# Kernel optimization log

Hardware: AMD Instinct MI355X
Metric: run time of the kernel (lower is better)

Reference implementation:

```python
import jax, jax.numpy as jnp
import numpy as np

N, E = 10000, 320000
NODE_DIM, EDGE_DIM, HID, H, L = 128, 64, 128, 4, 2
NEG_SLOPE = 0.2
BN_EPS = 1e-5


def setup_inputs() -> dict:
    key = jax.random.key(0)
    ks = jax.random.split(key, 20)
    s = 0.05
    return {
        "x": jax.random.normal(ks[0], (N, NODE_DIM), jnp.float32),
        "edge_index": jax.random.randint(ks[1], (2, E), 0, N, jnp.int32),
        "edge_attr": jax.random.normal(ks[2], (E, EDGE_DIM), jnp.float32),
        "batch": jnp.zeros((N,), jnp.int32),
        "enc_W": jax.random.normal(ks[3], (NODE_DIM, HID), jnp.float32) * s,
        "enc_b": jnp.zeros((HID,), jnp.float32),
        "eenc_W": jax.random.normal(ks[4], (EDGE_DIM, HID), jnp.float32) * s,
        "eenc_b": jnp.zeros((HID,), jnp.float32),
        "W": jax.random.normal(ks[5], (L, HID, H * HID), jnp.float32) * s,
        "We": jax.random.normal(ks[6], (L, HID, H * HID), jnp.float32) * s,
        "att_src": jax.random.normal(ks[7], (L, H, HID), jnp.float32) * s,
        "att_dst": jax.random.normal(ks[8], (L, H, HID), jnp.float32) * s,
        "att_edge": jax.random.normal(ks[9], (L, H, HID), jnp.float32) * s,
        "bias": jnp.zeros((L, HID), jnp.float32),
        "gamma": jnp.ones((L, HID), jnp.float32),
        "beta": jnp.zeros((L, HID), jnp.float32),
    }


def _forward(x, edge_attr, enc_W, enc_b, eenc_W, eenc_b, W, We,
             att_src, att_dst, att_edge, bias, gamma, beta, src, dst):
    h = x @ enc_W + enc_b                      # [N, HID]
    ea = edge_attr @ eenc_W + eenc_b           # [E, HID]
    # add self-loops; fill_value='mean' -> per-dst-node mean of incoming edge feats
    deg = jax.ops.segment_sum(jnp.ones((E,), ea.dtype), dst, N)          # [N]
    loop_attr = jax.ops.segment_sum(ea, dst, N) / jnp.maximum(deg, 1.0)[:, None]
    src_f = jnp.concatenate([src, jnp.arange(N, dtype=src.dtype)])       # [E+N]
    dst_f = jnp.concatenate([dst, jnp.arange(N, dtype=dst.dtype)])
    ea_f = jnp.concatenate([ea, loop_attr], axis=0)                      # [E+N, HID]

    for l in range(L):
        xh = (h @ W[l]).reshape(N, H, HID)                 # [N,H,C]
        eh = (ea_f @ We[l]).reshape(E + N, H, HID)         # [E+N,H,C]
        a_src = jnp.einsum('nhc,hc->nh', xh, att_src[l])   # [N,H]
        a_dst = jnp.einsum('nhc,hc->nh', xh, att_dst[l])
        a_e = jnp.einsum('ehc,hc->eh', eh, att_edge[l])    # [E+N,H]
        alpha = a_src[src_f] + a_dst[dst_f] + a_e
        alpha = jnp.where(alpha >= 0, alpha, NEG_SLOPE * alpha)  # leaky_relu
        amax = jax.ops.segment_max(alpha, dst_f, N)        # [N,H]
        alpha = jnp.exp(alpha - amax[dst_f])
        denom = jax.ops.segment_sum(alpha, dst_f, N)       # [N,H]
        alpha = alpha / (denom[dst_f] + 1e-16)
        msg = xh[src_f] * alpha[:, :, None]                # [E+N,H,C]
        out = jax.ops.segment_sum(msg, dst_f, N).mean(axis=1) + bias[l]  # concat=False -> head mean
        mu = out.mean(axis=0)
        var = out.var(axis=0)
        out = (out - mu) * jax.lax.rsqrt(var + BN_EPS) * gamma[l] + beta[l]
        h = jax.nn.relu(out) + h                           # relu, dropout(eval)=id, residual
    return h


def reference(x, edge_index, edge_attr, batch, enc_W, enc_b, eenc_W, eenc_b,
              W, We, att_src, att_dst, att_edge, bias, gamma, beta):
    src, dst = edge_index[0], edge_index[1]
    return _forward(x, edge_attr, enc_W, enc_b, eenc_W, eenc_b, W, We,
                    att_src, att_dst, att_edge, bias, gamma, beta, src, dst)
```

## Files before the change

kernel.cpp:

```cpp
#include <hip/hip_runtime.h>
#include <hip/hip_bf16.h>

typedef __attribute__((ext_vector_type(8))) short short8;
typedef __attribute__((ext_vector_type(4))) float f32x4;

__device__ __forceinline__ unsigned short f2bf(float x) {
    unsigned int u = __float_as_uint(x);
    u += 0x7fffu + ((u >> 16) & 1u);
    return (unsigned short)(u >> 16);
}

__device__ __forceinline__ unsigned int pack2(float a, float b) {
    return (unsigned int)f2bf(a) | ((unsigned int)f2bf(b) << 16);
}

__device__ __forceinline__ float2 bf2(unsigned int u) {
    float lo = __uint_as_float(u << 16);
    float hi = __uint_as_float(u & 0xffff0000u);
    return make_float2(lo, hi);
}

__global__ __launch_bounds__(256) void k_prep(const float* __restrict__ encW,
                                              const float* __restrict__ W,
                                              unsigned short* __restrict__ encWT16,
                                              unsigned short* __restrict__ WT16) {
    int o = blockIdx.x * 256 + threadIdx.x;
    if (o < 16384) {
        int c = o >> 7, k = o & 127;
        encWT16[o] = f2bf(encW[k * 128 + c]);
    } else if (o < 16384 + 131072) {
        int o2 = o - 16384;
        int l = o2 >> 16, r = o2 & 65535;
        int c = r >> 7, k = r & 127;
        WT16[o2] = f2bf(W[((size_t)l * 128 + k) * 512 + c]);
    }
}

__global__ __launch_bounds__(256) void k_wa(const float* __restrict__ W,
                                            const float* __restrict__ We,
                                            const float* __restrict__ att_src,
                                            const float* __restrict__ att_dst,
                                            const float* __restrict__ att_edge,
                                            float* __restrict__ we_att,
                                            float* __restrict__ wa_sd) {
    int o = blockIdx.x * 256 + threadIdx.x;
    if (o < 1024) {
        int k = o >> 3, lh = o & 7, l = lh >> 2, h = lh & 3;
        const float* wrow = We + ((size_t)(l * 128 + k)) * 512 + h * 128;
        const float* av = att_edge + (l * 4 + h) * 128;
        float s = 0.f;
        #pragma unroll 8
        for (int c = 0; c < 128; ++c) s = fmaf(wrow[c], av[c], s);
        we_att[o] = s;
    } else if (o < 3072) {
        int o2 = o - 1024;
        int l = o2 >> 10, r = o2 & 1023, k = r >> 3, m = r & 7, h = m & 3;
        const float* wrow = W + ((size_t)(l * 128 + k)) * 512 + h * 128;
        const float* av = (m < 4 ? att_src : att_dst) + (l * 4 + h) * 128;
        float s = 0.f;
        #pragma unroll 8
        for (int c = 0; c < 128; ++c) s = fmaf(wrow[c], av[c], s);
        wa_sd[o2] = s;
    }
}

__global__ __launch_bounds__(256) void k_mw(const float* __restrict__ eencW,
                                            const float* __restrict__ eencb,
                                            const float* __restrict__ we_att,
                                            float* __restrict__ MW,
                                            float* __restrict__ cvec) {
    int o = blockIdx.x * 256 + threadIdx.x;
    if (o < 512) {
        int k = o >> 3, q = o & 7;
        float s = 0.f;
        #pragma unroll 8
        for (int c = 0; c < 128; ++c) s = fmaf(eencW[k * 128 + c], we_att[c * 8 + q], s);
        MW[o] = s;
    } else if (o < 520) {
        int q = o - 512;
        float s = 0.f;
        #pragma unroll 8
        for (int c = 0; c < 128; ++c) s = fmaf(eencb[c], we_att[c * 8 + q], s);
        cvec[q] = s;
    }
}

template <int NC, bool A32, bool W32, bool W16, bool BIAS>
__global__ __launch_bounds__(256) void k_gemm_mfma(
    const void* __restrict__ A,
    const unsigned short* __restrict__ BT16,
    const float* __restrict__ bias,
    float* __restrict__ C,
    unsigned short* __restrict__ C16, int M) {
    __shared__ unsigned short a_lds[64][136];
    __shared__ unsigned short b_lds[64][136];
    int t = threadIdx.x;
    int rbase = blockIdx.x * 64;
    int cbase = blockIdx.y * 64;
    #pragma unroll
    for (int i = 0; i < 4; ++i) {
        int idx = t * 8 + i * 2048;
        int r = idx >> 7, k = idx & 127;
        if constexpr (A32) {
            const float* Af = (const float*)A;
            float4 f0 = make_float4(0.f, 0.f, 0.f, 0.f), f1 = f0;
            if (rbase + r < M) {
                f0 = *(const float4*)(Af + (size_t)(rbase + r) * 128 + k);
                f1 = *(const float4*)(Af + (size_t)(rbase + r) * 128 + k + 4);
            }
            uint4 v = make_uint4(pack2(f0.x, f0.y), pack2(f0.z, f0.w),
                                 pack2(f1.x, f1.y), pack2(f1.z, f1.w));
            *(uint4*)&a_lds[r][k] = v;
        } else {
            const unsigned short* Ah = (const unsigned short*)A;
            uint4 v = make_uint4(0u, 0u, 0u, 0u);
            if (rbase + r < M) v = *(const uint4*)(Ah + (size_t)(rbase + r) * 128 + k);
            *(uint4*)&a_lds[r][k] = v;
        }
    }
    #pragma unroll
    for (int i = 0; i < 4; ++i) {
        int idx = t * 8 + i * 2048;
        int r = idx >> 7, k = idx & 127;
        uint4 v = *(const uint4*)(BT16 + (size_t)(cbase + r) * 128 + k);
        *(uint4*)&b_lds[r][k] = v;
    }
    __syncthreads();
    int lane = t & 63, w = t >> 6;
    int lr = lane & 15, lk = (lane >> 4) * 8;
    f32x4 acc[4] = {f32x4{0.f, 0.f, 0.f, 0.f}, f32x4{0.f, 0.f, 0.f, 0.f},
                    f32x4{0.f, 0.f, 0.f, 0.f}, f32x4{0.f, 0.f, 0.f, 0.f}};
    #pragma unroll
    for (int kt = 0; kt < 4; ++kt) {
        short8 a = *(const short8*)&a_lds[w * 16 + lr][kt * 32 + lk];
        #pragma unroll
        for (int ct = 0; ct < 4; ++ct) {
            short8 b = *(const short8*)&b_lds[ct * 16 + lr][kt * 32 + lk];
            acc[ct] = __builtin_amdgcn_mfma_f32_16x16x32_bf16(a, b, acc[ct], 0, 0, 0);
        }
    }
    int rw = rbase + w * 16 + (lane >> 4) * 4;
    #pragma unroll
    for (int ct = 0; ct < 4; ++ct) {
        int col = cbase + ct * 16 + lr;
        float bv = 0.f;
        if constexpr (BIAS) bv = bias[col];
        #pragma unroll
        for (int j = 0; j < 4; ++j) {
            int r = rw + j;
            if (r < M) {
                float v = acc[ct][j] + bv;
                if constexpr (W32) C[(size_t)r * NC + col] = v;
                if constexpr (W16) C16[(size_t)r * NC + col] = f2bf(v);
            }
        }
    }
}

__global__ __launch_bounds__(256) void k_hist(const int* __restrict__ dst,
                                              int* __restrict__ deg, int E_) {
    int e = blockIdx.x * 256 + threadIdx.x;
    if (e < E_) atomicAdd(&deg[dst[e]], 1);
}

__global__ __launch_bounds__(1024) void k_scan(const int* __restrict__ deg,
                                               int* __restrict__ offs, int n) {
    __shared__ int part[1024];
    int t = threadIdx.x;
    int per = (n + 1023) / 1024;
    int beg = t * per, end = min(beg + per, n);
    int s = 0;
    for (int i = beg; i < end; ++i) s += deg[i];
    part[t] = s;
    __syncthreads();
    for (int off = 1; off < 1024; off <<= 1) {
        int v = (t >= off) ? part[t - off] : 0;
        __syncthreads();
        part[t] += v;
        __syncthreads();
    }
    int run = (t == 0) ? 0 : part[t - 1];
    for (int i = beg; i < end; ++i) { offs[i] = run; run += deg[i]; }
    if (t == 1023) offs[n] = run;
}

__global__ __launch_bounds__(256) void k_fill_ae(
    const int* __restrict__ dst, const int* __restrict__ src,
    const int* __restrict__ offs, int* __restrict__ fill,
    const float* __restrict__ eattr, const float* __restrict__ MW,
    const float* __restrict__ cvec,
    int* __restrict__ src_s, float* __restrict__ a_e_i, int E_) {
    __shared__ float mw[64][8];
    __shared__ float cv[8];
    int t = threadIdx.x;
    for (int i = t; i < 512; i += 256) mw[i >> 3][i & 7] = MW[i];
    if (t < 8) cv[t] = cvec[t];
    __syncthreads();
    int e = blockIdx.x * 256 + t;
    if (e >= E_) return;
    float acc[8];
    #pragma unroll
    for (int q = 0; q < 8; ++q) acc[q] = cv[q];
    const float4* r = (const float4*)(eattr + (size_t)e * 64);
    #pragma unroll 4
    for (int k4 = 0; k4 < 16; ++k4) {
        float4 v = r[k4];
        float xc[4] = {v.x, v.y, v.z, v.w};
        #pragma unroll
        for (int m = 0; m < 4; ++m)
            #pragma unroll
            for (int q = 0; q < 8; ++q)
                acc[q] = fmaf(xc[m], mw[k4 * 4 + m][q], acc[q]);
    }
    int d = dst[e];
    int pos = offs[d] + atomicAdd(&fill[d], 1);
    src_s[pos] = src[e];
    *(float4*)(a_e_i + (size_t)pos * 8) = make_float4(acc[0], acc[1], acc[2], acc[3]);
    *(float4*)(a_e_i + (size_t)pos * 8 + 4) = make_float4(acc[4], acc[5], acc[6], acc[7]);
}

__global__ __launch_bounds__(256) void k_rowdot8(const float* __restrict__ X,
                                                 const float* __restrict__ V,
                                                 float* __restrict__ O, int M) {
    __shared__ float v_lds[128][8];
    int t = threadIdx.x;
    for (int idx = t; idx < 1024; idx += 256) v_lds[idx >> 3][idx & 7] = V[idx];
    __syncthreads();
    int row = blockIdx.x * 256 + t;
    if (row >= M) return;
    float acc[8] = {};
    const float4* x4 = (const float4*)(X + (size_t)row * 128);
    for (int k4 = 0; k4 < 32; ++k4) {
        float4 xv = x4[k4];
        float xc[4] = {xv.x, xv.y, xv.z, xv.w};
        #pragma unroll
        for (int m = 0; m < 4; ++m)
            #pragma unroll
            for (int o = 0; o < 8; ++o) acc[o] = fmaf(xc[m], v_lds[k4 * 4 + m][o], acc[o]);
    }
    *(float4*)(O + (size_t)row * 8) = make_float4(acc[0], acc[1], acc[2], acc[3]);
    *(float4*)(O + (size_t)row * 8 + 4) = make_float4(acc[4], acc[5], acc[6], acc[7]);
}

__global__ __launch_bounds__(256) void k_agg(
    const int* __restrict__ offs, const int* __restrict__ src_s,
    const float* __restrict__ a_sd, const float* __restrict__ a_e_i,
    const unsigned short* __restrict__ xh16,
    float* __restrict__ outb, int N_, int lsel) {
    int wid = (blockIdx.x * 256 + threadIdx.x) >> 6;
    int lane = threadIdx.x & 63;
    if (wid >= N_) return;
    int n = wid;
    int s0 = offs[n], s1 = offs[n + 1];
    int hsel = lane >> 4;
    int qoff = lsel * 4 + hsel;
    float ad = a_sd[(size_t)n * 8 + 4 + hsel];
    float acc[8] = {};
    float ssum = 0.f, macc = 0.f;
    int sn_next = (s0 < s1) ? src_s[s0] : 0;
    for (int idx = s0; idx < s1; ++idx) {
        int sn = sn_next;
        if (idx + 1 < s1) sn_next = src_s[idx + 1];
        float ae = a_e_i[(size_t)idx * 8 + qoff];
        float as = a_sd[(size_t)sn * 8 + hsel];
        uint4 v = *(const uint4*)(xh16 + (size_t)sn * 512 + lane * 8);
        macc += ae;
        float raw = as + ae + ad;
        raw = raw >= 0.f ? raw : 0.2f * raw;
        float ex = __expf(raw);
        ssum += ex;
        float2 p0 = bf2(v.x), p1 = bf2(v.y), p2 = bf2(v.z), p3 = bf2(v.w);
        acc[0] = fmaf(ex, p0.x, acc[0]); acc[1] = fmaf(ex, p0.y, acc[1]);
        acc[2] = fmaf(ex, p1.x, acc[2]); acc[3] = fmaf(ex, p1.y, acc[3]);
        acc[4] = fmaf(ex, p2.x, acc[4]); acc[5] = fmaf(ex, p2.y, acc[5]);
        acc[6] = fmaf(ex, p3.x, acc[6]); acc[7] = fmaf(ex, p3.y, acc[7]);
    }
    {
        float dg = (float)max(s1 - s0, 1);
        float ae = macc / dg;
        float as = a_sd[(size_t)n * 8 + hsel];
        float raw = as + ae + ad;
        raw = raw >= 0.f ? raw : 0.2f * raw;
        float ex = __expf(raw);
        ssum += ex;
        uint4 v = *(const uint4*)(xh16 + (size_t)n * 512 + lane * 8);
        float2 p0 = bf2(v.x), p1 = bf2(v.y), p2 = bf2(v.z), p3 = bf2(v.w);
        acc[0] = fmaf(ex, p0.x, acc[0]); acc[1] = fmaf(ex, p0.y, acc[1]);
        acc[2] = fmaf(ex, p1.x, acc[2]); acc[3] = fmaf(ex, p1.y, acc[3]);
        acc[4] = fmaf(ex, p2.x, acc[4]); acc[5] = fmaf(ex, p2.y, acc[5]);
        acc[6] = fmaf(ex, p3.x, acc[6]); acc[7] = fmaf(ex, p3.y, acc[7]);
    }
    float inv = 0.25f / (ssum + 1e-16f);
    #pragma unroll
    for (int q = 0; q < 8; ++q) acc[q] *= inv;
    #pragma unroll
    for (int off = 16; off <= 32; off <<= 1)
        #pragma unroll
        for (int q = 0; q < 8; ++q) acc[q] += __shfl_xor(acc[q], off);
    if (lane < 16) {
        float* orow = outb + (size_t)n * 128 + lane * 8;
        *(float4*)orow = make_float4(acc[0], acc[1], acc[2], acc[3]);
        *(float4*)(orow + 4) = make_float4(acc[4], acc[5], acc[6], acc[7]);
    }
}

__global__ __launch_bounds__(128) void k_bnstats(const float* __restrict__ outb,
                                                 float* __restrict__ bnsum,
                                                 float* __restrict__ bnsumsq, int N_) {
    int c = threadIdx.x;
    float s = 0.f, s2 = 0.f;
    for (int r = blockIdx.x; r < N_; r += gridDim.x) {
        float v = outb[(size_t)r * 128 + c];
        s += v;
        s2 = fmaf(v, v, s2);
    }
    atomicAdd(&bnsum[c], s);
    atomicAdd(&bnsumsq[c], s2);
}

template <bool DOROW>
__global__ __launch_bounds__(256) void k_bn_apply_rd(
    const float* __restrict__ outb, const float* __restrict__ bnsum,
    const float* __restrict__ bnsumsq, const float* __restrict__ gamma,
    const float* __restrict__ beta, const float* __restrict__ wa,
    float* __restrict__ h, unsigned short* __restrict__ h16,
    float* __restrict__ a_sd, int N_) {
    __shared__ float wlds[128][8];
    int t = threadIdx.x;
    if constexpr (DOROW) {
        for (int i = t; i < 1024; i += 256) wlds[i >> 3][i & 7] = wa[i];
        __syncthreads();
    }
    int wid = (blockIdx.x * 256 + t) >> 6;
    int lane = t & 63;
    if (wid >= N_) return;
    int n = wid;
    float invN = 1.0f / (float)N_;
    int c0 = lane, c1 = lane + 64;
    float mu0 = bnsum[c0] * invN, mu1 = bnsum[c1] * invN;
    float g0 = rsqrtf(bnsumsq[c0] * invN - mu0 * mu0 + 1e-5f) * gamma[c0];
    float g1 = rsqrtf(bnsumsq[c1] * invN - mu1 * mu1 + 1e-5f) * gamma[c1];
    float o0 = outb[(size_t)n * 128 + c0], o1 = outb[(size_t)n * 128 + c1];
    float v0 = (o0 - mu0) * g0 + beta[c0];
    float v1 = (o1 - mu1) * g1 + beta[c1];
    float nh0 = h[(size_t)n * 128 + c0] + fmaxf(v0, 0.f);
    float nh1 = h[(size_t)n * 128 + c1] + fmaxf(v1, 0.f);
    h[(size_t)n * 128 + c0] = nh0;
    h[(size_t)n * 128 + c1] = nh1;
    h16[(size_t)n * 128 + c0] = f2bf(nh0);
    h16[(size_t)n * 128 + c1] = f2bf(nh1);
    if constexpr (DOROW) {
        float p[8];
        #pragma unroll
        for (int m = 0; m < 8; ++m)
            p[m] = fmaf(nh0, wlds[c0][m], nh1 * wlds[c1][m]);
        #pragma unroll
        for (int off = 1; off < 64; off <<= 1)
            #pragma unroll
            for (int m = 0; m < 8; ++m) p[m] += __shfl_xor(p[m], off);
        if (lane == 0) {
            *(float4*)(a_sd + (size_t)n * 8) = make_float4(p[0], p[1], p[2], p[3]);
            *(float4*)(a_sd + (size_t)n * 8 + 4) = make_float4(p[4], p[5], p[6], p[7]);
        }
    }
}

extern "C" void kernel_launch(void* const* d_in, const int* in_sizes, int n_in,
                              void* d_out, int out_size, void* d_ws, size_t ws_size,
                              hipStream_t stream) {
    const float* x = (const float*)d_in[0];
    const int* ei = (const int*)d_in[1];
    const float* eattr = (const float*)d_in[2];
    const float* encW = (const float*)d_in[4];
    const float* encb = (const float*)d_in[5];
    const float* eencW = (const float*)d_in[6];
    const float* eencb = (const float*)d_in[7];
    const float* W = (const float*)d_in[8];
    const float* We = (const float*)d_in[9];
    const float* att_src = (const float*)d_in[10];
    const float* att_dst = (const float*)d_in[11];
    const float* att_edge = (const float*)d_in[12];
    const float* gamma = (const float*)d_in[14];
    const float* beta = (const float*)d_in[15];

    const int N = in_sizes[0] / 128;
    const int E = in_sizes[1] / 2;
    const int* srcIdx = ei;
    const int* dstIdx = ei + E;
    float* h = (float*)d_out;

    char* wbase = (char*)d_ws;
    size_t off = 0;
    auto alloc = [&](size_t bytes) -> void* {
        void* p = wbase + off;
        off = (off + bytes + 255) & ~(size_t)255;
        return p;
    };
    unsigned short* encWT16 = (unsigned short*)alloc((size_t)128 * 128 * 2);
    unsigned short* WT16 = (unsigned short*)alloc((size_t)2 * 512 * 128 * 2);
    float* we_att = (float*)alloc((size_t)128 * 8 * 4);
    float* wa_sd = (float*)alloc((size_t)2 * 128 * 8 * 4);
    float* MW = (float*)alloc((size_t)64 * 8 * 4);
    float* cvec = (float*)alloc((size_t)8 * 4);
    int* deg = (int*)alloc((size_t)2 * N * 4);
    int* fill = deg + N;
    int* offs = (int*)alloc((size_t)(N + 1) * 4);
    int* src_s = (int*)alloc((size_t)E * 4);
    float* a_e_i = (float*)alloc((size_t)E * 8 * 4);
    float* a_sd = (float*)alloc((size_t)N * 8 * 4);
    unsigned short* h16 = (unsigned short*)alloc((size_t)N * 128 * 2);
    unsigned short* xh16 = (unsigned short*)alloc((size_t)N * 512 * 2);
    float* outb = (float*)alloc((size_t)N * 128 * 4);
    float* bnsum = (float*)alloc((size_t)4 * 128 * 4);
    float* bnsumsq = bnsum + 2 * 128;
    (void)ws_size; (void)n_in; (void)out_size;

    hipMemsetAsync(deg, 0, (size_t)2 * N * 4, stream);
    hipMemsetAsync(bnsum, 0, (size_t)4 * 128 * 4, stream);

    k_prep<<<(16384 + 131072 + 255) / 256, 256, 0, stream>>>(encW, W, encWT16, WT16);
    k_wa<<<12, 256, 0, stream>>>(W, We, att_src, att_dst, att_edge, we_att, wa_sd);
    k_mw<<<3, 256, 0, stream>>>(eencW, eencb, we_att, MW, cvec);

    k_gemm_mfma<128, true, true, true, true>
        <<<dim3((N + 63) / 64, 2), 256, 0, stream>>>(x, encWT16, encb, h, h16, N);

    int eb = (E + 255) / 256;
    k_hist<<<eb, 256, 0, stream>>>(dstIdx, deg, E);
    k_scan<<<1, 1024, 0, stream>>>(deg, offs, N);
    k_fill_ae<<<eb, 256, 0, stream>>>(dstIdx, srcIdx, offs, fill, eattr, MW, cvec,
                                      src_s, a_e_i, E);

    k_rowdot8<<<(N + 255) / 256, 256, 0, stream>>>(h, wa_sd, a_sd, N);

    int ab = (N * 64 + 255) / 256;
    for (int l = 0; l < 2; ++l) {
        k_gemm_mfma<512, false, false, true, false>
            <<<dim3((N + 63) / 64, 8), 256, 0, stream>>>(
                h16, WT16 + (size_t)l * 512 * 128, nullptr, nullptr, xh16, N);
        k_agg<<<ab, 256, 0, stream>>>(
            offs, src_s, a_sd, a_e_i, xh16, outb, N, l);
        k_bnstats<<<256, 128, 0, stream>>>(outb, bnsum + l * 128, bnsumsq + l * 128, N);
        if (l == 0) {
            k_bn_apply_rd<true><<<ab, 256, 0, stream>>>(
                outb, bnsum, bnsumsq, gamma, beta, wa_sd + 1024, h, h16, a_sd, N);
        } else {
            k_bn_apply_rd<false><<<ab, 256, 0, stream>>>(
                outb, bnsum + 128, bnsumsq + 128, gamma + 128, beta + 128,
                nullptr, h, h16, nullptr, N);
        }
    }
}
```

Measured before the change: 272.0 us.

## Merge setup kernels into fewer launches and unroll aggregation loop by two

Combines the weight prep, attention-weight folding and degree histogram into one launch, runs the scan alongside the MW computation in a two-block launch, and merges edge fill with the source/dest row dot into one launch. This removes several small kernel launches and the gaps between them. The aggregation loop now handles two edges per iteration with separate accumulators, which raises memory-level parallelism at the cost of more registers.

```diff
diff --git a/kernel.cpp b/kernel.cpp
--- a/kernel.cpp
+++ b/kernel.cpp
@@ -20,69 +20,90 @@
     return make_float2(lo, hi);
 }
 
-__global__ __launch_bounds__(256) void k_prep(const float* __restrict__ encW,
-                                              const float* __restrict__ W,
-                                              unsigned short* __restrict__ encWT16,
-                                              unsigned short* __restrict__ WT16) {
-    int o = blockIdx.x * 256 + threadIdx.x;
-    if (o < 16384) {
-        int c = o >> 7, k = o & 127;
-        encWT16[o] = f2bf(encW[k * 128 + c]);
-    } else if (o < 16384 + 131072) {
-        int o2 = o - 16384;
-        int l = o2 >> 16, r = o2 & 65535;
-        int c = r >> 7, k = r & 127;
-        WT16[o2] = f2bf(W[((size_t)l * 128 + k) * 512 + c]);
-    }
-}
-
-__global__ __launch_bounds__(256) void k_wa(const float* __restrict__ W,
-                                            const float* __restrict__ We,
-                                            const float* __restrict__ att_src,
-                                            const float* __restrict__ att_dst,
-                                            const float* __restrict__ att_edge,
-                                            float* __restrict__ we_att,
-                                            float* __restrict__ wa_sd) {
-    int o = blockIdx.x * 256 + threadIdx.x;
-    if (o < 1024) {
-        int k = o >> 3, lh = o & 7, l = lh >> 2, h = lh & 3;
-        const float* wrow = We + ((size_t)(l * 128 + k)) * 512 + h * 128;
-        const float* av = att_edge + (l * 4 + h) * 128;
-        float s = 0.f;
-        #pragma unroll 8
-        for (int c = 0; c < 128; ++c) s = fmaf(wrow[c], av[c], s);
-        we_att[o] = s;
-    } else if (o < 3072) {
-        int o2 = o - 1024;
-        int l = o2 >> 10, r = o2 & 1023, k = r >> 3, m = r & 7, h = m & 3;
-        const float* wrow = W + ((size_t)(l * 128 + k)) * 512 + h * 128;
-        const float* av = (m < 4 ? att_src : att_dst) + (l * 4 + h) * 128;
-        float s = 0.f;
-        #pragma unroll 8
-        for (int c = 0; c < 128; ++c) s = fmaf(wrow[c], av[c], s);
-        wa_sd[o2] = s;
-    }
-}
-
-__global__ __launch_bounds__(256) void k_mw(const float* __restrict__ eencW,
-                                            const float* __restrict__ eencb,
-                                            const float* __restrict__ we_att,
-                                            float* __restrict__ MW,
-                                            float* __restrict__ cvec) {
-    int o = blockIdx.x * 256 + threadIdx.x;
-    if (o < 512) {
-        int k = o >> 3, q = o & 7;
-        float s = 0.f;
-        #pragma unroll 8
-        for (int c = 0; c < 128; ++c) s = fmaf(eencW[k * 128 + c], we_att[c * 8 + q], s);
-        MW[o] = s;
-    } else if (o < 520) {
-        int q = o - 512;
-        float s = 0.f;
-        #pragma unroll 8
-        for (int c = 0; c < 128; ++c) s = fmaf(eencb[c], we_att[c * 8 + q], s);
-        cvec[q] = s;
-    }
+__global__ __launch_bounds__(256) void k_misc1(
+    const float* __restrict__ encW, const float* __restrict__ W,
+    const float* __restrict__ We, const float* __restrict__ att_src,
+    const float* __restrict__ att_dst, const float* __restrict__ att_edge,
+    const int* __restrict__ dst,
+    unsigned short* __restrict__ encWT16, unsigned short* __restrict__ WT16,
+    float* __restrict__ we_att, float* __restrict__ wa_sd,
+    int* __restrict__ deg, int E_) {
+    int b = blockIdx.x, t = threadIdx.x;
+    if (b < 576) {
+        int o = b * 256 + t;
+        if (o < 16384) {
+            int c = o >> 7, k = o & 127;
+            encWT16[o] = f2bf(encW[k * 128 + c]);
+        } else {
+            int o2 = o - 16384;
+            int l = o2 >> 16, r = o2 & 65535;
+            int c = r >> 7, k = r & 127;
+            WT16[o2] = f2bf(W[((size_t)l * 128 + k) * 512 + c]);
+        }
+    } else if (b < 588) {
+        int o = (b - 576) * 256 + t;
+        if (o < 1024) {
+            int k = o >> 3, lh = o & 7, l = lh >> 2, hh = lh & 3;
+            const float* wrow = We + ((size_t)(l * 128 + k)) * 512 + hh * 128;
+            const float* av = att_edge + (l * 4 + hh) * 128;
+            float s = 0.f;
+            #pragma unroll 8
+            for (int c = 0; c < 128; ++c) s = fmaf(wrow[c], av[c], s);
+            we_att[o] = s;
+        } else if (o < 3072) {
+            int o2 = o - 1024;
+            int l = o2 >> 10, r = o2 & 1023, k = r >> 3, m = r & 7, hh = m & 3;
+            const float* wrow = W + ((size_t)(l * 128 + k)) * 512 + hh * 128;
+            const float* av = (m < 4 ? att_src : att_dst) + (l * 4 + hh) * 128;
+            float s = 0.f;
+            #pragma unroll 8
+            for (int c = 0; c < 128; ++c) s = fmaf(wrow[c], av[c], s);
+            wa_sd[o2] = s;
+        }
+    } else {
+        int e = (b - 588) * 256 + t;
+        if (e < E_) atomicAdd(&deg[dst[e]], 1);
+    }
+}
+
+__global__ __launch_bounds__(1024) void k_scan_mw(
+    const int* __restrict__ deg, int* __restrict__ offs, int n,
+    const float* __restrict__ eencW, const float* __restrict__ eencb,
+    const float* __restrict__ we_att,
+    float* __restrict__ MW, float* __restrict__ cvec) {
+    int t = threadIdx.x;
+    if (blockIdx.x == 1) {
+        if (t < 512) {
+            int k = t >> 3, q = t & 7;
+            float s = 0.f;
+            #pragma unroll 8
+            for (int c = 0; c < 128; ++c) s = fmaf(eencW[k * 128 + c], we_att[c * 8 + q], s);
+            MW[t] = s;
+        } else if (t < 520) {
+            int q = t - 512;
+            float s = 0.f;
+            #pragma unroll 8
+            for (int c = 0; c < 128; ++c) s = fmaf(eencb[c], we_att[c * 8 + q], s);
+            cvec[q] = s;
+        }
+        return;
+    }
+    __shared__ int part[1024];
+    int per = (n + 1023) / 1024;
+    int beg = t * per, end = min(beg + per, n);
+    int s = 0;
+    for (int i = beg; i < end; ++i) s += deg[i];
+    part[t] = s;
+    __syncthreads();
+    for (int off = 1; off < 1024; off <<= 1) {
+        int v = (t >= off) ? part[t - off] : 0;
+        __syncthreads();
+        part[t] += v;
+        __syncthreads();
+    }
+    int run = (t == 0) ? 0 : part[t - 1];
+    for (int i = beg; i < end; ++i) { offs[i] = run; run += deg[i]; }
+    if (t == 1023) offs[n] = run;
 }
 
 template <int NC, bool A32, bool W32, bool W16, bool BIAS>
@@ -157,89 +178,61 @@
     }
 }
 
-__global__ __launch_bounds__(256) void k_hist(const int* __restrict__ dst,
-                                              int* __restrict__ deg, int E_) {
-    int e = blockIdx.x * 256 + threadIdx.x;
-    if (e < E_) atomicAdd(&deg[dst[e]], 1);
-}
-
-__global__ __launch_bounds__(1024) void k_scan(const int* __restrict__ deg,
-                                               int* __restrict__ offs, int n) {
-    __shared__ int part[1024];
-    int t = threadIdx.x;
-    int per = (n + 1023) / 1024;
-    int beg = t * per, end = min(beg + per, n);
-    int s = 0;
-    for (int i = beg; i < end; ++i) s += deg[i];
-    part[t] = s;
-    __syncthreads();
-    for (int off = 1; off < 1024; off <<= 1) {
-        int v = (t >= off) ? part[t - off] : 0;
-        __syncthreads();
-        part[t] += v;
-        __syncthreads();
-    }
-    int run = (t == 0) ? 0 : part[t - 1];
-    for (int i = beg; i < end; ++i) { offs[i] = run; run += deg[i]; }
-    if (t == 1023) offs[n] = run;
-}
-
-__global__ __launch_bounds__(256) void k_fill_ae(
+__global__ __launch_bounds__(256) void k_fill_rd(
     const int* __restrict__ dst, const int* __restrict__ src,
     const int* __restrict__ offs, int* __restrict__ fill,
     const float* __restrict__ eattr, const float* __restrict__ MW,
     const float* __restrict__ cvec,
-    int* __restrict__ src_s, float* __restrict__ a_e_i, int E_) {
-    __shared__ float mw[64][8];
-    __shared__ float cv[8];
+    int* __restrict__ src_s, float* __restrict__ a_e_i, int E_,
+    const float* __restrict__ X, const float* __restrict__ V,
+    float* __restrict__ O, int M, int fillBlocks) {
     int t = threadIdx.x;
-    for (int i = t; i < 512; i += 256) mw[i >> 3][i & 7] = MW[i];
-    if (t < 8) cv[t] = cvec[t];
-    __syncthreads();
-    int e = blockIdx.x * 256 + t;
-    if (e >= E_) return;
-    float acc[8];
-    #pragma unroll
-    for (int q = 0; q < 8; ++q) acc[q] = cv[q];
-    const float4* r = (const float4*)(eattr + (size_t)e * 64);
-    #pragma unroll 4
-    for (int k4 = 0; k4 < 16; ++k4) {
-        float4 v = r[k4];
-        float xc[4] = {v.x, v.y, v.z, v.w};
-        #pragma unroll
-        for (int m = 0; m < 4; ++m)
+    if ((int)blockIdx.x < fillBlocks) {
+        __shared__ float mw[64][8];
+        __shared__ float cv[8];
+        for (int i = t; i < 512; i += 256) mw[i >> 3][i & 7] = MW[i];
+        if (t < 8) cv[t] = cvec[t];
+        __syncthreads();
+        int e = blockIdx.x * 256 + t;
+        if (e >= E_) return;
+        float acc[8];
+        #pragma unroll
+        for (int q = 0; q < 8; ++q) acc[q] = cv[q];
+        const float4* r = (const float4*)(eattr + (size_t)e * 64);
+        #pragma unroll 4
+        for (int k4 = 0; k4 < 16; ++k4) {
+            float4 v = r[k4];
+            float xc[4] = {v.x, v.y, v.z, v.w};
             #pragma unroll
-            for (int q = 0; q < 8; ++q)
-                acc[q] = fmaf(xc[m], mw[k4 * 4 + m][q], acc[q]);
-    }
-    int d = dst[e];
-    int pos = offs[d] + atomicAdd(&fill[d], 1);
-    src_s[pos] = src[e];
-    *(float4*)(a_e_i + (size_t)pos * 8) = make_float4(acc[0], acc[1], acc[2], acc[3]);
-    *(float4*)(a_e_i + (size_t)pos * 8 + 4) = make_float4(acc[4], acc[5], acc[6], acc[7]);
-}
-
-__global__ __launch_bounds__(256) void k_rowdot8(const float* __restrict__ X,
-                                                 const float* __restrict__ V,
-                                                 float* __restrict__ O, int M) {
-    __shared__ float v_lds[128][8];
-    int t = threadIdx.x;
-    for (int idx = t; idx < 1024; idx += 256) v_lds[idx >> 3][idx & 7] = V[idx];
-    __syncthreads();
-    int row = blockIdx.x * 256 + t;
-    if (row >= M) return;
-    float acc[8] = {};
-    const float4* x4 = (const float4*)(X + (size_t)row * 128);
-    for (int k4 = 0; k4 < 32; ++k4) {
-        float4 xv = x4[k4];
-        float xc[4] = {xv.x, xv.y, xv.z, xv.w};
-        #pragma unroll
-        for (int m = 0; m < 4; ++m)
+            for (int m = 0; m < 4; ++m)
+                #pragma unroll
+                for (int q = 0; q < 8; ++q)
+                    acc[q] = fmaf(xc[m], mw[k4 * 4 + m][q], acc[q]);
+        }
+        int d = dst[e];
+        int pos = offs[d] + atomicAdd(&fill[d], 1);
+        src_s[pos] = src[e];
+        *(float4*)(a_e_i + (size_t)pos * 8) = make_float4(acc[0], acc[1], acc[2], acc[3]);
+        *(float4*)(a_e_i + (size_t)pos * 8 + 4) = make_float4(acc[4], acc[5], acc[6], acc[7]);
+    } else {
+        __shared__ float v_lds[128][8];
+        for (int idx = t; idx < 1024; idx += 256) v_lds[idx >> 3][idx & 7] = V[idx];
+        __syncthreads();
+        int row = (blockIdx.x - fillBlocks) * 256 + t;
+        if (row >= M) return;
+        float acc[8] = {};
+        const float4* x4 = (const float4*)(X + (size_t)row * 128);
+        for (int k4 = 0; k4 < 32; ++k4) {
+            float4 xv = x4[k4];
+            float xc[4] = {xv.x, xv.y, xv.z, xv.w};
             #pragma unroll
-            for (int o = 0; o < 8; ++o) acc[o] = fmaf(xc[m], v_lds[k4 * 4 + m][o], acc[o]);
-    }
-    *(float4*)(O + (size_t)row * 8) = make_float4(acc[0], acc[1], acc[2], acc[3]);
-    *(float4*)(O + (size_t)row * 8 + 4) = make_float4(acc[4], acc[5], acc[6], acc[7]);
+            for (int m = 0; m < 4; ++m)
+                #pragma unroll
+                for (int o = 0; o < 8; ++o) acc[o] = fmaf(xc[m], v_lds[k4 * 4 + m][o], acc[o]);
+        }
+        *(float4*)(O + (size_t)row * 8) = make_float4(acc[0], acc[1], acc[2], acc[3]);
+        *(float4*)(O + (size_t)row * 8 + 4) = make_float4(acc[4], acc[5], acc[6], acc[7]);
+    }
 }
 
 __global__ __launch_bounds__(256) void k_agg(
@@ -255,12 +248,41 @@
     int hsel = lane >> 4;
     int qoff = lsel * 4 + hsel;
     float ad = a_sd[(size_t)n * 8 + 4 + hsel];
-    float acc[8] = {};
-    float ssum = 0.f, macc = 0.f;
-    int sn_next = (s0 < s1) ? src_s[s0] : 0;
-    for (int idx = s0; idx < s1; ++idx) {
-        int sn = sn_next;
-        if (idx + 1 < s1) sn_next = src_s[idx + 1];
+    float acc[8] = {}, acc2[8] = {};
+    float ssum = 0.f, ssum2 = 0.f, macc = 0.f;
+    int idx = s0;
+    int sa_n = 0, sb_n = 0;
+    if (idx + 1 < s1) { sa_n = src_s[idx]; sb_n = src_s[idx + 1]; }
+    for (; idx + 1 < s1; idx += 2) {
+        int sa = sa_n, sb = sb_n;
+        if (idx + 3 < s1) { sa_n = src_s[idx + 2]; sb_n = src_s[idx + 3]; }
+        float aea = a_e_i[(size_t)idx * 8 + qoff];
+        float aeb = a_e_i[(size_t)(idx + 1) * 8 + qoff];
+        float asa = a_sd[(size_t)sa * 8 + hsel];
+        float asb = a_sd[(size_t)sb * 8 + hsel];
+        uint4 va = *(const uint4*)(xh16 + (size_t)sa * 512 + lane * 8);
+        uint4 vb = *(const uint4*)(xh16 + (size_t)sb * 512 + lane * 8);
+        macc += aea + aeb;
+        float ra = asa + aea + ad;
+        ra = ra >= 0.f ? ra : 0.2f * ra;
+        float rb = asb + aeb + ad;
+        rb = rb >= 0.f ? rb : 0.2f * rb;
+        float exa = __expf(ra), exb = __expf(rb);
+        ssum += exa;
+        ssum2 += exb;
+        float2 a0 = bf2(va.x), a1 = bf2(va.y), a2 = bf2(va.z), a3 = bf2(va.w);
+        float2 b0 = bf2(vb.x), b1 = bf2(vb.y), b2 = bf2(vb.z), b3 = bf2(vb.w);
+        acc[0] = fmaf(exa, a0.x, acc[0]);  acc[1] = fmaf(exa, a0.y, acc[1]);
+        acc[2] = fmaf(exa, a1.x, acc[2]);  acc[3] = fmaf(exa, a1.y, acc[3]);
+        acc[4] = fmaf(exa, a2.x, acc[4]);  acc[5] = fmaf(exa, a2.y, acc[5]);
+        acc[6] = fmaf(exa, a3.x, acc[6]);  acc[7] = fmaf(exa, a3.y, acc[7]);
+        acc2[0] = fmaf(exb, b0.x, acc2[0]); acc2[1] = fmaf(exb, b0.y, acc2[1]);
+        acc2[2] = fmaf(exb, b1.x, acc2[2]); acc2[3] = fmaf(exb, b1.y, acc2[3]);
+        acc2[4] = fmaf(exb, b2.x, acc2[4]); acc2[5] = fmaf(exb, b2.y, acc2[5]);
+        acc2[6] = fmaf(exb, b3.x, acc2[6]); acc2[7] = fmaf(exb, b3.y, acc2[7]);
+    }
+    if (idx < s1) {
+        int sn = src_s[idx];
         float ae = a_e_i[(size_t)idx * 8 + qoff];
         float as = a_sd[(size_t)sn * 8 + hsel];
         uint4 v = *(const uint4*)(xh16 + (size_t)sn * 512 + lane * 8);
@@ -275,6 +297,9 @@
         acc[4] = fmaf(ex, p2.x, acc[4]); acc[5] = fmaf(ex, p2.y, acc[5]);
         acc[6] = fmaf(ex, p3.x, acc[6]); acc[7] = fmaf(ex, p3.y, acc[7]);
     }
+    ssum += ssum2;
+    #pragma unroll
+    for (int q = 0; q < 8; ++q) acc[q] += acc2[q];
     {
         float dg = (float)max(s1 - s0, 1);
         float ae = macc / dg;
@@ -418,20 +443,19 @@
     hipMemsetAsync(deg, 0, (size_t)2 * N * 4, stream);
     hipMemsetAsync(bnsum, 0, (size_t)4 * 128 * 4, stream);
 
-    k_prep<<<(16384 + 131072 + 255) / 256, 256, 0, stream>>>(encW, W, encWT16, WT16);
-    k_wa<<<12, 256, 0, stream>>>(W, We, att_src, att_dst, att_edge, we_att, wa_sd);
-    k_mw<<<3, 256, 0, stream>>>(eencW, eencb, we_att, MW, cvec);
+    int eb = (E + 255) / 256;
+    k_misc1<<<588 + eb, 256, 0, stream>>>(encW, W, We, att_src, att_dst, att_edge,
+                                          dstIdx, encWT16, WT16, we_att, wa_sd,
+                                          deg, E);
+    k_scan_mw<<<2, 1024, 0, stream>>>(deg, offs, N, eencW, eencb, we_att, MW, cvec);
 
     k_gemm_mfma<128, true, true, true, true>
         <<<dim3((N + 63) / 64, 2), 256, 0, stream>>>(x, encWT16, encb, h, h16, N);
 
-    int eb = (E + 255) / 256;
-    k_hist<<<eb, 256, 0, stream>>>(dstIdx, deg, E);
-    k_scan<<<1, 1024, 0, stream>>>(deg, offs, N);
-    k_fill_ae<<<eb, 256, 0, stream>>>(dstIdx, srcIdx, offs, fill, eattr, MW, cvec,
-                                      src_s, a_e_i, E);
-
-    k_rowdot8<<<(N + 255) / 256, 256, 0, stream>>>(h, wa_sd, a_sd, N);
+    int rb = (N + 255) / 256;
+    k_fill_rd<<<eb + rb, 256, 0, stream>>>(dstIdx, srcIdx, offs, fill, eattr, MW,
+                                           cvec, src_s, a_e_i, E, h, wa_sd, a_sd,
+                                           N, eb);
 
     int ab = (N * 64 + 255) / 256;
     for (int l = 0; l < 2; ++l) {
```

After: 243.1 us. 10.6% less time.
